# Optimization experiments

Hardware: AMD Instinct MI355X
Metric: run time of the kernel (lower is better)

## Reference

```python
import jax, jax.numpy as jnp
import numpy as np

B, IN, OUT = 256, 512, 512


def setup_inputs() -> dict:
    key = jax.random.key(0)
    k0, k1, k2, k3, k4, k5 = jax.random.split(key, 6)
    x_mean = jax.random.normal(k0, (B, IN), jnp.float32)
    x_var = jax.random.normal(k1, (B, IN, IN), jnp.float32)
    # params (original inits A_mean to zeros which gives a degenerate test;
    # use small random values for a meaningful numerical baseline)
    xavier_std = float(np.sqrt(2.0 / (IN + OUT)))
    A_mean = jax.random.normal(k2, (IN, OUT), jnp.float32) * xavier_std
    A_var = jax.random.normal(k3, (IN, OUT), jnp.float32) * xavier_std
    b_mean = jax.random.normal(k4, (OUT,), jnp.float32) * 0.01
    b_var = jax.random.normal(k5, (OUT,), jnp.float32)
    return {"x_mean": x_mean, "x_var": x_var, "A_mean": A_mean,
            "A_var": A_var, "b_mean": b_mean, "b_var": b_var}


def reference(x_mean, x_var, A_mean, A_var, b_mean, b_var):
    # y_mean = x A_mean + b_mean   (F.linear(x, A.t()) == x @ A)
    y_mean = x_mean @ A_mean + b_mean  # [B, OUT]

    # E[x x] diagonal: Var[x]_ii + mean_i^2
    x_var_diag = jnp.diagonal(x_var, axis1=1, axis2=2)  # [B, IN]
    xx_mean = x_var_diag + x_mean * x_mean
    term1_diag = xx_mean @ A_var  # [B, OUT]

    # A^T Cov[x] A, full matrix as in original, then take its diagonal
    xCov_A = jnp.einsum('bij,jo->bio', x_var, A_mean)      # [B, IN, OUT]
    A_xCov_A = jnp.einsum('bio,ip->bop', xCov_A, A_mean)   # [B, OUT, OUT]
    term2_diag = jnp.diagonal(A_xCov_A, axis1=1, axis2=2)  # [B, OUT]

    result_diag = term1_diag + term2_diag + b_var
    y_var = jax.vmap(jnp.diag)(result_diag)  # diag_embed -> [B, OUT, OUT]
    return y_mean, y_var
```

## Files before the change

### kernel.cpp

```cpp
#include <hip/hip_runtime.h>
#include <hip/hip_bf16.h>


typedef __bf16 bf16x8 __attribute__((ext_vector_type(8)));
typedef float f32x4 __attribute__((ext_vector_type(4)));

__device__ inline ushort f2bf(float f) {
    union { float f; unsigned u; } x; x.f = f;
    unsigned u = x.u + 0x7fffu + ((x.u >> 16) & 1u);
    return (ushort)(u >> 16);
}

__device__ inline void gload16(const void* g, void* l) {
    __builtin_amdgcn_global_load_lds(
        (const __attribute__((address_space(1))) void*)g,
        (__attribute__((address_space(3))) void*)l, 16, 0, 0);
}

__global__ void k_prep_at(const float* __restrict__ am, ushort* __restrict__ abt) {
    int C = blockIdx.x * 256 + threadIdx.x;
    int nt = C >> 13;
    int L  = C & 8191;
    int ks = L >> 10;
    int rem = L & 1023;
    int r = rem >> 3, cs = rem & 7;
    int c = cs ^ (r & 7);
    int o = nt * 128 + r;
    int j0 = ks * 64 + c * 8;
    ushort u[8];
    #pragma unroll
    for (int e = 0; e < 8; ++e) u[e] = f2bf(am[(j0 + e) * 512 + o]);
    *(int4*)(abt + (long)C * 8) = *(int4*)u;
}

__global__ void k_diag(const float* __restrict__ xv, const float* __restrict__ xm,
                       float* __restrict__ xx) {
    int idx = blockIdx.x * 256 + threadIdx.x;
    int b = idx >> 9, i = idx & 511;
    float m = xm[idx];
    xx[idx] = xv[(long)b * 262144 + i * 513] + m * m;
}

__global__ void k_t1(const float* __restrict__ xm, const float* __restrict__ xx,
                     const float* __restrict__ am, const float* __restrict__ av,
                     float* __restrict__ yp, float* __restrict__ tp) {
    __shared__ float S[2][64];
    int t = threadIdx.x;
    int b  = blockIdx.x >> 3;
    int ic = blockIdx.x & 7;
    int i0 = ic * 64;
    if (t < 128) {
        int which = t >> 6, ii = t & 63;
        const float* src = which ? xx : xm;
        S[which][ii] = src[b * 512 + i0 + ii];
    }
    __syncthreads();
    int mat = t >> 7;
    int o4 = t & 127;
    const float* M = mat ? av : am;
    const float* Sv = S[mat];
    f32x4 acc = {0.f, 0.f, 0.f, 0.f};
    #pragma unroll 8
    for (int ii = 0; ii < 64; ++ii) {
        f32x4 a = *(const f32x4*)(M + (long)(i0 + ii) * 512 + o4 * 4);
        float s = Sv[ii];
        acc[0] = fmaf(s, a[0], acc[0]);
        acc[1] = fmaf(s, a[1], acc[1]);
        acc[2] = fmaf(s, a[2], acc[2]);
        acc[3] = fmaf(s, a[3], acc[3]);
    }
    float* dst = (mat ? tp : yp) + ((long)ic * 256 + b) * 512 + o4 * 4;
    *(f32x4*)dst = acc;
}

__global__ __launch_bounds__(256, 3) void k_gemm2(
        const float*  __restrict__ xv,
        const ushort* __restrict__ abt,
        const float*  __restrict__ amean,
        float* __restrict__ p2,
        float* __restrict__ yvar)
{
    __shared__ float  ldsX[8192];
    __shared__ ushort ldsA[8192];
    __shared__ float  red[2][128];

    int t = threadIdx.x;
    int lane = t & 63;
    int wave = t >> 6;
    int wm = wave >> 1, wn = wave & 1;

    int bid = blockIdx.x;
    int swz = (bid & 7) * 512 + (bid >> 3);
    int mtile = swz >> 2;
    int ntile = swz & 3;
    int n0 = ntile * 128;
    long m0 = (long)mtile * 128;
    int msub = mtile & 3;
    int b = mtile >> 2;

    f32x4 acc[4][4];
    #pragma unroll
    for (int a = 0; a < 4; ++a)
        #pragma unroll
        for (int bq = 0; bq < 4; ++bq)
            acc[a][bq] = (f32x4){0.f, 0.f, 0.f, 0.f};

    int rl = lane >> 4;
    int cle = (lane & 15) ^ rl;
    const float* xb_e = xv + (m0 + wave * 32 + rl) * 512 + cle * 4;
    const float* xb_o = xv + (m0 + wave * 32 + 4 + rl) * 512 + (cle ^ 4) * 4;

    auto stageX = [&](int ks) {
        char* xd = (char*)ldsX + wave * 8192;
        #pragma unroll
        for (int q = 0; q < 8; q += 2) {
            gload16(xb_e + ks * 64 + q * 4 * 512, xd + q * 1024);
            gload16(xb_o + ks * 64 + q * 4 * 512, xd + (q + 1) * 1024);
        }
    };
    const char* asrc = (const char*)abt + (long)ntile * 131072
                       + wave * 4096 + (lane << 4);
    auto stageA = [&](int ks) {
        char* ad = (char*)ldsA + wave * 4096;
        const char* s = asrc + ks * 16384;
        #pragma unroll
        for (int q = 0; q < 4; ++q)
            gload16(s + q * 1024, ad + q * 1024);
    };

    float* zb = yvar + ((long)b * 512 + msub * 128 + ntile * 32) * 512 + t * 4;

    auto compute = [&](int kc) {
        bf16x8 af[4], bfr[4];
        int g = lane >> 4;
        int kb = kc * 64 + g * 16;
        #pragma unroll
        for (int nf = 0; nf < 4; ++nf) {
            int r = wn * 64 + nf * 16 + (lane & 15);
            bfr[nf] = *(const bf16x8*)((const char*)ldsA + r * 128
                                       + (kb ^ ((r & 7) << 4)));
        }
        #pragma unroll
        for (int mf = 0; mf < 4; ++mf) {
            int r = wm * 64 + mf * 16 + (lane & 15);
            int sw = r & 7;
            const char* bx = (const char*)ldsX + r * 256 + kc * 128;
            f32x4 lo = *(const f32x4*)(bx + (((2 * g) ^ sw) << 4));
            f32x4 hi = *(const f32x4*)(bx + (((2 * g + 1) ^ sw) << 4));
            bf16x8 a;
            a[0] = (__bf16)lo[0]; a[1] = (__bf16)lo[1];
            a[2] = (__bf16)lo[2]; a[3] = (__bf16)lo[3];
            a[4] = (__bf16)hi[0]; a[5] = (__bf16)hi[1];
            a[6] = (__bf16)hi[2]; a[7] = (__bf16)hi[3];
            af[mf] = a;
        }
        #pragma unroll
        for (int mf = 0; mf < 4; ++mf)
            #pragma unroll
            for (int nf = 0; nf < 4; ++nf)
                acc[mf][nf] = __builtin_amdgcn_mfma_f32_16x16x32_bf16(
                    af[mf], bfr[nf], acc[mf][nf], 0, 0, 0);
    };

    for (int ks = 0; ks < 8; ++ks) {
        stageX(ks);
        stageA(ks);
        __syncthreads();
        compute(0);
        compute(1);
        __syncthreads();
    }

    {
        float4 z = make_float4(0.f, 0.f, 0.f, 0.f);
        #pragma unroll
        for (int q = 0; q < 16; ++q)
            *(float4*)(zb + (long)q * 1024) = z;
    }

    #pragma unroll
    for (int nf = 0; nf < 4; ++nf) {
        float p = 0.f;
        int o = n0 + wn * 64 + nf * 16 + (lane & 15);
        #pragma unroll
        for (int mf = 0; mf < 4; ++mf) {
            #pragma unroll
            for (int j = 0; j < 4; ++j) {
                int i = msub * 128 + wm * 64 + mf * 16 + ((lane >> 4) * 4) + j;
                p += acc[mf][nf][j] * amean[i * 512 + o];
            }
        }
        p += __shfl_xor(p, 16, 64);
        p += __shfl_xor(p, 32, 64);
        if (lane < 16) red[wm][wn * 64 + nf * 16 + lane] = p;
    }
    __syncthreads();
    if (t < 128) {
        float v = red[0][t] + red[1][t];
        p2[((long)b * 4 + msub) * 512 + n0 + t] = v;
    }
}

__global__ void k_final(const float* __restrict__ yp, const float* __restrict__ tp,
                        const float* __restrict__ p2,
                        const float* __restrict__ bm, const float* __restrict__ bv,
                        float* __restrict__ ymean, float* __restrict__ yvar) {
    int idx = blockIdx.x * 256 + threadIdx.x;
    int b = idx >> 9, o = idx & 511;
    float ym = bm[o], t1 = bv[o];
    #pragma unroll
    for (int ic = 0; ic < 8; ++ic) {
        ym += yp[((long)ic * 256 + b) * 512 + o];
        t1 += tp[((long)ic * 256 + b) * 512 + o];
    }
    long pb = (long)b * 2048 + o;
    t1 += p2[pb] + p2[pb + 512] + p2[pb + 1024] + p2[pb + 1536];
    ymean[idx] = ym;
    yvar[(long)idx * 512 + o] = t1;
}

extern "C" void kernel_launch(void* const* d_in, const int* in_sizes, int n_in,
                              void* d_out, int out_size, void* d_ws, size_t ws_size,
                              hipStream_t stream) {
    const float* x_mean = (const float*)d_in[0];
    const float* x_var  = (const float*)d_in[1];
    const float* A_mean = (const float*)d_in[2];
    const float* A_var  = (const float*)d_in[3];
    const float* b_mean = (const float*)d_in[4];
    const float* b_var  = (const float*)d_in[5];

    float* ymean = (float*)d_out;
    float* yvar  = (float*)d_out + 131072;

    char* ws = (char*)d_ws;
    ushort* abt = (ushort*)ws;
    float*  p2  = (float*)(ws + 512 * 1024);
    float*  yp  = (float*)(ws + 2560 * 1024);
    float*  tp  = (float*)(ws + 6656 * 1024);
    float*  xx  = (float*)(ws + 10752 * 1024);

    k_prep_at<<<128, 256, 0, stream>>>(A_mean, abt);
    k_diag<<<512, 256, 0, stream>>>(x_var, x_mean, xx);
    k_t1<<<2048, 256, 0, stream>>>(x_mean, xx, A_mean, A_var, yp, tp);
    k_gemm2<<<4096, 256, 0, stream>>>(x_var, abt, A_mean, p2, yvar);
    k_final<<<512, 256, 0, stream>>>(yp, tp, p2, b_mean, b_var, ymean, yvar);
}
```

Baseline: 202.9 us.

## Double-buffer LDS staging in gemm2 with half-size K steps and async waits

Splits the gemm2 K loop into 16 steps of 32 and double-buffers both the X and A tiles in LDS. The next tile's global-to-LDS loads are issued before computing the current one, with vmcnt waits and raw barriers in place of __syncthreads. The prep kernel's packed A layout and swizzle change to match the new 32-wide K chunks, and the yvar zero-fill moves after the reduction. The aim is to hide global load latency behind MFMA work. Total LDS stays the same, but the code now depends on exact vmcnt counts and the new swizzle being correct.

```diff
diff --git a/kernel.cpp b/kernel.cpp
--- a/kernel.cpp
+++ b/kernel.cpp
@@ -21,12 +21,14 @@
     int C = blockIdx.x * 256 + threadIdx.x;
     int nt = C >> 13;
     int L  = C & 8191;
-    int ks = L >> 10;
-    int rem = L & 1023;
-    int r = rem >> 3, cs = rem & 7;
-    int c = cs ^ (r & 7);
+    int ks = L >> 9;
+    int rem = L & 511;
+    int s = rem >> 3, c = rem & 7;
+    int lc = c ^ (s & 7);
+    int h = lc >> 2, g = lc & 3;
+    int r = 2 * s + h;
     int o = nt * 128 + r;
-    int j0 = ks * 64 + c * 8;
+    int j0 = ks * 32 + g * 8;
     ushort u[8];
     #pragma unroll
     for (int e = 0; e < 8; ++e) u[e] = f2bf(am[(j0 + e) * 512 + o]);
@@ -80,8 +82,8 @@
         float* __restrict__ p2,
         float* __restrict__ yvar)
 {
-    __shared__ float  ldsX[8192];
-    __shared__ ushort ldsA[8192];
+    __shared__ float  ldsX[2][4096];
+    __shared__ ushort ldsA[2][4096];
     __shared__ float  red[2][128];
 
     int t = threadIdx.x;
@@ -105,46 +107,39 @@
         for (int bq = 0; bq < 4; ++bq)
             acc[a][bq] = (f32x4){0.f, 0.f, 0.f, 0.f};
 
-    int rl = lane >> 4;
-    int cle = (lane & 15) ^ rl;
-    const float* xb_e = xv + (m0 + wave * 32 + rl) * 512 + cle * 4;
-    const float* xb_o = xv + (m0 + wave * 32 + 4 + rl) * 512 + (cle ^ 4) * 4;
-
-    auto stageX = [&](int ks) {
-        char* xd = (char*)ldsX + wave * 8192;
-        #pragma unroll
-        for (int q = 0; q < 8; q += 2) {
-            gload16(xb_e + ks * 64 + q * 4 * 512, xd + q * 1024);
-            gload16(xb_o + ks * 64 + q * 4 * 512, xd + (q + 1) * 1024);
-        }
+    const float* xs0 = xv + (m0 + wave * 32 + (lane >> 3)) * 512
+                       + ((lane & 7) ^ (lane >> 3)) * 4;
+    const char* as0 = (const char*)abt + (long)ntile * 131072
+                      + wave * 2048 + lane * 16;
+
+    auto stage = [&](int buf, int ks) {
+        char* xd = (char*)(&ldsX[buf][0]) + wave * 4096;
+        const float* sx = xs0 + ks * 32;
+        #pragma unroll
+        for (int q = 0; q < 4; ++q)
+            gload16(sx + q * 8 * 512, xd + q * 1024);
+        char* ad = (char*)(&ldsA[buf][0]) + wave * 2048;
+        const char* sa = as0 + (long)ks * 8192;
+        gload16(sa, ad);
+        gload16(sa + 1024, ad + 1024);
     };
-    const char* asrc = (const char*)abt + (long)ntile * 131072
-                       + wave * 4096 + (lane << 4);
-    auto stageA = [&](int ks) {
-        char* ad = (char*)ldsA + wave * 4096;
-        const char* s = asrc + ks * 16384;
-        #pragma unroll
-        for (int q = 0; q < 4; ++q)
-            gload16(s + q * 1024, ad + q * 1024);
-    };
-
-    float* zb = yvar + ((long)b * 512 + msub * 128 + ntile * 32) * 512 + t * 4;
-
-    auto compute = [&](int kc) {
+
+    auto compute = [&](int buf) {
         bf16x8 af[4], bfr[4];
         int g = lane >> 4;
-        int kb = kc * 64 + g * 16;
         #pragma unroll
         for (int nf = 0; nf < 4; ++nf) {
             int r = wn * 64 + nf * 16 + (lane & 15);
-            bfr[nf] = *(const bf16x8*)((const char*)ldsA + r * 128
-                                       + (kb ^ ((r & 7) << 4)));
+            int s = r >> 1;
+            int chunk = (((r & 1) << 2) | g) ^ (s & 7);
+            bfr[nf] = *(const bf16x8*)((const char*)(&ldsA[buf][0])
+                                       + s * 128 + (chunk << 4));
         }
         #pragma unroll
         for (int mf = 0; mf < 4; ++mf) {
             int r = wm * 64 + mf * 16 + (lane & 15);
             int sw = r & 7;
-            const char* bx = (const char*)ldsX + r * 256 + kc * 128;
+            const char* bx = (const char*)(&ldsX[buf][0]) + r * 128;
             f32x4 lo = *(const f32x4*)(bx + (((2 * g) ^ sw) << 4));
             f32x4 hi = *(const f32x4*)(bx + (((2 * g + 1) ^ sw) << 4));
             bf16x8 a;
@@ -162,20 +157,19 @@
                     af[mf], bfr[nf], acc[mf][nf], 0, 0, 0);
     };
 
-    for (int ks = 0; ks < 8; ++ks) {
-        stageX(ks);
-        stageA(ks);
-        __syncthreads();
-        compute(0);
-        compute(1);
-        __syncthreads();
-    }
-
-    {
-        float4 z = make_float4(0.f, 0.f, 0.f, 0.f);
-        #pragma unroll
-        for (int q = 0; q < 16; ++q)
-            *(float4*)(zb + (long)q * 1024) = z;
+    stage(0, 0);
+    int cur = 0;
+    #pragma unroll
+    for (int ks = 0; ks < 16; ++ks) {
+        if (ks < 15) stage(cur ^ 1, ks + 1);
+        if (ks < 15) asm volatile("s_waitcnt vmcnt(6)" ::: "memory");
+        else         asm volatile("s_waitcnt vmcnt(0)" ::: "memory");
+        __builtin_amdgcn_s_barrier();
+        __builtin_amdgcn_sched_barrier(0);
+        compute(cur);
+        __builtin_amdgcn_sched_barrier(0);
+        __builtin_amdgcn_s_barrier();
+        cur ^= 1;
     }
 
     #pragma unroll
@@ -199,6 +193,14 @@
         float v = red[0][t] + red[1][t];
         p2[((long)b * 4 + msub) * 512 + n0 + t] = v;
     }
+
+    {
+        float* zb = yvar + ((long)b * 512 + msub * 128 + ntile * 32) * 512 + t * 4;
+        float4 z = make_float4(0.f, 0.f, 0.f, 0.f);
+        #pragma unroll
+        for (int q = 0; q < 16; ++q)
+            *(float4*)(zb + (long)q * 1024) = z;
+    }
 }
 
 __global__ void k_final(const float* __restrict__ yp, const float* __restrict__ tp,
```

Result: slower. 220.7 us (+8.8%).

## Double-buffer GEMM with register-staged bf16 X and split out zero fill

Applied to the files above, without the earlier changes.

Rewrites the main GEMM kernel to use 512 threads with double-buffered LDS. X tiles are loaded into registers two steps ahead, converted to bf16 and written to LDS while the current buffer is being computed. A_mean tiles are prefetched one step ahead through global-to-LDS loads. Zeroing of the large y_var output moves into a separate fill kernel, and storing X as bf16 halves its LDS footprint. The aim is to overlap global loads with MFMA work and remove the per-step double barrier, at the cost of more registers, manual waitcnt tuning, and an extra kernel launch.

```diff
diff --git a/kernel.cpp b/kernel.cpp
--- a/kernel.cpp
+++ b/kernel.cpp
@@ -3,6 +3,7 @@
 
 
 typedef __bf16 bf16x8 __attribute__((ext_vector_type(8)));
+typedef __bf16 bf16x4 __attribute__((ext_vector_type(4)));
 typedef float f32x4 __attribute__((ext_vector_type(4)));
 
 __device__ inline ushort f2bf(float f) {
@@ -73,21 +74,29 @@
     *(f32x4*)dst = acc;
 }
 
-__global__ __launch_bounds__(256, 3) void k_gemm2(
+__global__ void k_fillz(float* __restrict__ yvar) {
+    int idx = blockIdx.x * 256 + threadIdx.x;
+    float4 z = make_float4(0.f, 0.f, 0.f, 0.f);
+    #pragma unroll 8
+    for (int k = 0; k < 32; ++k)
+        *(float4*)(yvar + ((long)k * 524288 + idx) * 4) = z;
+}
+
+__global__ __launch_bounds__(512, 4) void k_gemm2(
         const float*  __restrict__ xv,
         const ushort* __restrict__ abt,
         const float*  __restrict__ amean,
-        float* __restrict__ p2,
-        float* __restrict__ yvar)
+        float* __restrict__ p2)
 {
-    __shared__ float  ldsX[8192];
-    __shared__ ushort ldsA[8192];
-    __shared__ float  red[2][128];
+    __shared__ ushort ldsX[2][8192];
+    __shared__ ushort ldsA[2][8192];
+    __shared__ float  red[4][128];
 
     int t = threadIdx.x;
     int lane = t & 63;
-    int wave = t >> 6;
-    int wm = wave >> 1, wn = wave & 1;
+    int w = t >> 6;
+    int wm = w >> 1, wn = w & 1;
+    int rl = lane & 15, g = lane >> 4;
 
     int bid = blockIdx.x;
     int swz = (bid & 7) * 512 + (bid >> 3);
@@ -98,95 +107,117 @@
     int msub = mtile & 3;
     int b = mtile >> 2;
 
-    f32x4 acc[4][4];
-    #pragma unroll
-    for (int a = 0; a < 4; ++a)
-        #pragma unroll
-        for (int bq = 0; bq < 4; ++bq)
-            acc[a][bq] = (f32x4){0.f, 0.f, 0.f, 0.f};
-
-    int rl = lane >> 4;
-    int cle = (lane & 15) ^ rl;
-    const float* xb_e = xv + (m0 + wave * 32 + rl) * 512 + cle * 4;
-    const float* xb_o = xv + (m0 + wave * 32 + 4 + rl) * 512 + (cle ^ 4) * 4;
-
-    auto stageX = [&](int ks) {
-        char* xd = (char*)ldsX + wave * 8192;
-        #pragma unroll
-        for (int q = 0; q < 8; q += 2) {
-            gload16(xb_e + ks * 64 + q * 4 * 512, xd + q * 1024);
-            gload16(xb_o + ks * 64 + q * 4 * 512, xd + (q + 1) * 1024);
-        }
-    };
-    const char* asrc = (const char*)abt + (long)ntile * 131072
-                       + wave * 4096 + (lane << 4);
-    auto stageA = [&](int ks) {
-        char* ad = (char*)ldsA + wave * 4096;
-        const char* s = asrc + ks * 16384;
-        #pragma unroll
-        for (int q = 0; q < 4; ++q)
-            gload16(s + q * 1024, ad + q * 1024);
-    };
-
-    float* zb = yvar + ((long)b * 512 + msub * 128 + ntile * 32) * 512 + t * 4;
-
-    auto compute = [&](int kc) {
-        bf16x8 af[4], bfr[4];
-        int g = lane >> 4;
-        int kb = kc * 64 + g * 16;
-        #pragma unroll
-        for (int nf = 0; nf < 4; ++nf) {
-            int r = wn * 64 + nf * 16 + (lane & 15);
-            bfr[nf] = *(const bf16x8*)((const char*)ldsA + r * 128
-                                       + (kb ^ ((r & 7) << 4)));
-        }
-        #pragma unroll
-        for (int mf = 0; mf < 4; ++mf) {
-            int r = wm * 64 + mf * 16 + (lane & 15);
-            int sw = r & 7;
-            const char* bx = (const char*)ldsX + r * 256 + kc * 128;
-            f32x4 lo = *(const f32x4*)(bx + (((2 * g) ^ sw) << 4));
-            f32x4 hi = *(const f32x4*)(bx + (((2 * g + 1) ^ sw) << 4));
-            bf16x8 a;
-            a[0] = (__bf16)lo[0]; a[1] = (__bf16)lo[1];
-            a[2] = (__bf16)lo[2]; a[3] = (__bf16)lo[3];
-            a[4] = (__bf16)hi[0]; a[5] = (__bf16)hi[1];
-            a[6] = (__bf16)hi[2]; a[7] = (__bf16)hi[3];
-            af[mf] = a;
-        }
-        #pragma unroll
-        for (int mf = 0; mf < 4; ++mf)
-            #pragma unroll
-            for (int nf = 0; nf < 4; ++nf)
-                acc[mf][nf] = __builtin_amdgcn_mfma_f32_16x16x32_bf16(
-                    af[mf], bfr[nf], acc[mf][nf], 0, 0, 0);
-    };
-
+    f32x4 acc[2][4];
+    #pragma unroll
+    for (int mf = 0; mf < 2; ++mf)
+        #pragma unroll
+        for (int nf = 0; nf < 4; ++nf)
+            acc[mf][nf] = (f32x4){0.f, 0.f, 0.f, 0.f};
+
+    const float* xbase = xv + (m0 + w * 16 + g) * 512 + rl * 4;
+    const char*  abase = (const char*)abt + (long)ntile * 131072 + w * 2048 + lane * 16;
+
+    float4 xA[4], xB[4];
+
+    auto loadXA = [&](int ks) {
+        #pragma unroll
+        for (int j = 0; j < 4; ++j)
+            xA[j] = *(const float4*)(xbase + (long)j * 2048 + ks * 64);
+    };
+    auto loadXB = [&](int ks) {
+        #pragma unroll
+        for (int j = 0; j < 4; ++j)
+            xB[j] = *(const float4*)(xbase + (long)j * 2048 + ks * 64);
+    };
+    auto gldsA = [&](int buf, int ks) {
+        const char* src = abase + (long)ks * 16384;
+        char* dst = (char*)ldsA[buf] + w * 2048;
+        gload16(src, dst);
+        gload16(src + 1024, dst + 1024);
+    };
+    auto writeXA = [&](int buf) {
+        #pragma unroll
+        for (int j = 0; j < 4; ++j) {
+            int r = w * 16 + j * 4 + g;
+            bf16x4 v;
+            v[0] = (__bf16)xA[j].x; v[1] = (__bf16)xA[j].y;
+            v[2] = (__bf16)xA[j].z; v[3] = (__bf16)xA[j].w;
+            int off = r * 128 + (((rl >> 1) << 4) ^ ((r & 7) << 4)) + (rl & 1) * 8;
+            *(bf16x4*)((char*)ldsX[buf] + off) = v;
+        }
+    };
+    auto writeXB = [&](int buf) {
+        #pragma unroll
+        for (int j = 0; j < 4; ++j) {
+            int r = w * 16 + j * 4 + g;
+            bf16x4 v;
+            v[0] = (__bf16)xB[j].x; v[1] = (__bf16)xB[j].y;
+            v[2] = (__bf16)xB[j].z; v[3] = (__bf16)xB[j].w;
+            int off = r * 128 + (((rl >> 1) << 4) ^ ((r & 7) << 4)) + (rl & 1) * 8;
+            *(bf16x4*)((char*)ldsX[buf] + off) = v;
+        }
+    };
+    auto compute = [&](int buf) {
+        #pragma unroll
+        for (int kc = 0; kc < 2; ++kc) {
+            bf16x8 af[2], bfr[4];
+            int kb = kc * 64 + g * 16;
+            #pragma unroll
+            for (int mf = 0; mf < 2; ++mf) {
+                int r = wm * 32 + mf * 16 + rl;
+                af[mf] = *(const bf16x8*)((const char*)ldsX[buf] + r * 128
+                                          + (kb ^ ((r & 7) << 4)));
+            }
+            #pragma unroll
+            for (int nf = 0; nf < 4; ++nf) {
+                int r = wn * 64 + nf * 16 + rl;
+                bfr[nf] = *(const bf16x8*)((const char*)ldsA[buf] + r * 128
+                                           + (kb ^ ((r & 7) << 4)));
+            }
+            #pragma unroll
+            for (int mf = 0; mf < 2; ++mf)
+                #pragma unroll
+                for (int nf = 0; nf < 4; ++nf)
+                    acc[mf][nf] = __builtin_amdgcn_mfma_f32_16x16x32_bf16(
+                        af[mf], bfr[nf], acc[mf][nf], 0, 0, 0);
+        }
+    };
+
+    gldsA(0, 0);
+    loadXA(0);
+    writeXA(0);
+    loadXB(1);
+    asm volatile("s_waitcnt vmcnt(4) lgkmcnt(0)" ::: "memory");
+    __builtin_amdgcn_s_barrier();
+    __builtin_amdgcn_sched_barrier(0);
+
+    #pragma unroll
     for (int ks = 0; ks < 8; ++ks) {
-        stageX(ks);
-        stageA(ks);
-        __syncthreads();
-        compute(0);
-        compute(1);
-        __syncthreads();
-    }
-
-    {
-        float4 z = make_float4(0.f, 0.f, 0.f, 0.f);
-        #pragma unroll
-        for (int q = 0; q < 16; ++q)
-            *(float4*)(zb + (long)q * 1024) = z;
+        const int p = ks & 1;
+        if (ks <= 6) gldsA(1 - p, ks + 1);
+        if (ks <= 5) { if (p == 0) loadXA(ks + 2); else loadXB(ks + 2); }
+        compute(p);
+        if (ks <= 6) { if (p == 0) writeXB(1 - p); else writeXA(1 - p); }
+        if (ks <= 5) {
+            asm volatile("s_waitcnt vmcnt(4) lgkmcnt(0)" ::: "memory");
+            __builtin_amdgcn_s_barrier();
+            __builtin_amdgcn_sched_barrier(0);
+        } else if (ks == 6) {
+            asm volatile("s_waitcnt vmcnt(0) lgkmcnt(0)" ::: "memory");
+            __builtin_amdgcn_s_barrier();
+            __builtin_amdgcn_sched_barrier(0);
+        }
     }
 
     #pragma unroll
     for (int nf = 0; nf < 4; ++nf) {
         float p = 0.f;
-        int o = n0 + wn * 64 + nf * 16 + (lane & 15);
-        #pragma unroll
-        for (int mf = 0; mf < 4; ++mf) {
+        int o = n0 + wn * 64 + nf * 16 + rl;
+        #pragma unroll
+        for (int mf = 0; mf < 2; ++mf) {
             #pragma unroll
             for (int j = 0; j < 4; ++j) {
-                int i = msub * 128 + wm * 64 + mf * 16 + ((lane >> 4) * 4) + j;
+                int i = msub * 128 + wm * 32 + mf * 16 + g * 4 + j;
                 p += acc[mf][nf][j] * amean[i * 512 + o];
             }
         }
@@ -196,7 +227,7 @@
     }
     __syncthreads();
     if (t < 128) {
-        float v = red[0][t] + red[1][t];
+        float v = red[0][t] + red[1][t] + red[2][t] + red[3][t];
         p2[((long)b * 4 + msub) * 512 + n0 + t] = v;
     }
 }
@@ -240,8 +271,9 @@
     float*  xx  = (float*)(ws + 10752 * 1024);
 
     k_prep_at<<<128, 256, 0, stream>>>(A_mean, abt);
+    k_fillz<<<2048, 256, 0, stream>>>(yvar);
     k_diag<<<512, 256, 0, stream>>>(x_var, x_mean, xx);
     k_t1<<<2048, 256, 0, stream>>>(x_mean, xx, A_mean, A_var, yp, tp);
-    k_gemm2<<<4096, 256, 0, stream>>>(x_var, abt, A_mean, p2, yvar);
+    k_gemm2<<<4096, 512, 0, stream>>>(x_var, abt, A_mean, p2);
     k_final<<<512, 256, 0, stream>>>(yp, tp, p2, b_mean, b_var, ymean, yvar);
 }
```

Result: slower. 273.0 us (+34.6%).
